# Kernel optimization log

Measured on AMD Instinct MI355X. Metric: run time of the kernel, lower is better.

Reference implementation:

```python
import jax, jax.numpy as jnp
import numpy as np

EPS = 1e-8


def setup_inputs() -> dict:
    key = jax.random.key(0)
    k1, k2, k3 = jax.random.split(key, 3)
    B, N_in, C = 4, 49152, 64   # 12*4^6 source cells
    N_out, K = 196608, 4        # 12*4^7 target cells, 4 IDW neighbors
    x = jax.random.normal(k1, (B, N_in, C), dtype=jnp.float32)
    nn_idx = jax.random.randint(k2, (N_out, K), 0, N_in, dtype=jnp.int64)
    nn_dist = jax.random.uniform(k3, (N_out, K), dtype=jnp.float32)
    return {"x": x, "nn_idx": nn_idx, "nn_dist": nn_dist}


def reference(x, nn_idx, nn_dist):
    # Inverse-distance weights over K nearest neighbors, normalized per target cell.
    inv = 1.0 / (nn_dist + EPS)                      # [N_out, K]
    w = inv / jnp.sum(inv, axis=-1, keepdims=True)   # [N_out, K]
    gathered = x[:, nn_idx, :]                       # [B, N_out, K, C] gather along source cells
    out = jnp.einsum("bnkc,nk->bnc", gathered, w)    # weighted reduce over neighbors
    return out
```

## Files before the change

kernel.cpp:

```cpp
#include <hip/hip_runtime.h>


#define IWD_EPS 1e-8f

typedef float f32x4 __attribute__((ext_vector_type(4)));
typedef int   i32x4 __attribute__((ext_vector_type(4)));
typedef unsigned int u32x4 __attribute__((ext_vector_type(4)));
typedef unsigned int u32x2 __attribute__((ext_vector_type(2)));

__device__ __forceinline__ float bf16lo_to_f32(unsigned int v) {
    unsigned int b = v << 16;
    return __builtin_bit_cast(float, b);
}
__device__ __forceinline__ float bf16hi_to_f32(unsigned int v) {
    unsigned int b = v & 0xFFFF0000u;
    return __builtin_bit_cast(float, b);
}
__device__ __forceinline__ unsigned int f32_to_bf16_rne(float f) {
    unsigned int u = __builtin_bit_cast(unsigned int, f);
    u += 0x7FFFu + ((u >> 16) & 1u);
    return u >> 16;
}

__global__ __launch_bounds__(256) void iwd_convert_bf16_kernel(
    const float* __restrict__ x, unsigned short* __restrict__ xb16, int nvec8)
{
    const int i = blockIdx.x * blockDim.x + threadIdx.x;
    if (i >= nvec8) return;
    const f32x4 a = *reinterpret_cast<const f32x4*>(x + (size_t)i * 8);
    const f32x4 b = *reinterpret_cast<const f32x4*>(x + (size_t)i * 8 + 4);
    u32x4 p;
    p.x = f32_to_bf16_rne(a.x) | (f32_to_bf16_rne(a.y) << 16);
    p.y = f32_to_bf16_rne(a.z) | (f32_to_bf16_rne(a.w) << 16);
    p.z = f32_to_bf16_rne(b.x) | (f32_to_bf16_rne(b.y) << 16);
    p.w = f32_to_bf16_rne(b.z) | (f32_to_bf16_rne(b.w) << 16);
    __builtin_nontemporal_store(p, reinterpret_cast<u32x4*>(xb16 + (size_t)i * 8));
}

__global__ __launch_bounds__(256) void IWD_ProjLayer_65876208386401_kernel(
    const unsigned short* __restrict__ xb16,
    const int*   __restrict__ nn_idx,
    const float* __restrict__ nn_dist,
    float* __restrict__ out)
{
    constexpr int N_in  = 49152;
    constexpr int C     = 64;
    constexpr int N_out = 196608;

    const int bid   = blockIdx.x;
    const int xcd   = bid & 7;
    const int b     = xcd >> 1;
    const int chunk = ((bid >> 3) << 1) | (xcd & 1);

    const int n  = chunk * 16 + (threadIdx.x >> 4);
    const int cq = (threadIdx.x & 15) * 4;

    const f32x4 d4 = *reinterpret_cast<const f32x4*>(nn_dist + (size_t)n * 4);
    const i32x4 id = *reinterpret_cast<const i32x4*>(nn_idx + (size_t)n * 4);

    const float i0 = 1.0f / (d4.x + IWD_EPS);
    const float i1 = 1.0f / (d4.y + IWD_EPS);
    const float i2 = 1.0f / (d4.z + IWD_EPS);
    const float i3 = 1.0f / (d4.w + IWD_EPS);
    const float r  = 1.0f / (i0 + i1 + i2 + i3);
    const float w0 = i0 * r, w1 = i1 * r, w2 = i2 * r, w3 = i3 * r;

    const unsigned short* xb = xb16 + (size_t)b * N_in * C;
    const u32x2 a0 = *reinterpret_cast<const u32x2*>(xb + (size_t)id.x * C + cq);
    const u32x2 a1 = *reinterpret_cast<const u32x2*>(xb + (size_t)id.y * C + cq);
    const u32x2 a2 = *reinterpret_cast<const u32x2*>(xb + (size_t)id.z * C + cq);
    const u32x2 a3 = *reinterpret_cast<const u32x2*>(xb + (size_t)id.w * C + cq);

    f32x4 o;
    o.x = bf16lo_to_f32(a0.x) * w0 + bf16lo_to_f32(a1.x) * w1
        + bf16lo_to_f32(a2.x) * w2 + bf16lo_to_f32(a3.x) * w3;
    o.y = bf16hi_to_f32(a0.x) * w0 + bf16hi_to_f32(a1.x) * w1
        + bf16hi_to_f32(a2.x) * w2 + bf16hi_to_f32(a3.x) * w3;
    o.z = bf16lo_to_f32(a0.y) * w0 + bf16lo_to_f32(a1.y) * w1
        + bf16lo_to_f32(a2.y) * w2 + bf16lo_to_f32(a3.y) * w3;
    o.w = bf16hi_to_f32(a0.y) * w0 + bf16hi_to_f32(a1.y) * w1
        + bf16hi_to_f32(a2.y) * w2 + bf16hi_to_f32(a3.y) * w3;

    __builtin_nontemporal_store(
        o, reinterpret_cast<f32x4*>(out + ((size_t)b * N_out + n) * C + cq));
}

__global__ __launch_bounds__(256) void iwd_f32_fallback_kernel(
    const float* __restrict__ x, const int* __restrict__ nn_idx,
    const float* __restrict__ nn_dist, float* __restrict__ out)
{
    constexpr int N_in = 49152, C = 64, N_out = 196608;
    const int bid = blockIdx.x, xcd = bid & 7, b = xcd >> 1;
    const int chunk = ((bid >> 3) << 1) | (xcd & 1);
    const int n  = chunk * 16 + (threadIdx.x >> 4);
    const int cq = (threadIdx.x & 15) * 4;

    const f32x4 d4 = *reinterpret_cast<const f32x4*>(nn_dist + (size_t)n * 4);
    const i32x4 id = *reinterpret_cast<const i32x4*>(nn_idx + (size_t)n * 4);
    const float i0 = 1.0f / (d4.x + IWD_EPS), i1 = 1.0f / (d4.y + IWD_EPS);
    const float i2 = 1.0f / (d4.z + IWD_EPS), i3 = 1.0f / (d4.w + IWD_EPS);
    const float r = 1.0f / (i0 + i1 + i2 + i3);
    const float w0 = i0 * r, w1 = i1 * r, w2 = i2 * r, w3 = i3 * r;

    const float* xb = x + (size_t)b * N_in * C;
    const f32x4 a0 = *reinterpret_cast<const f32x4*>(xb + (size_t)id.x * C + cq);
    const f32x4 a1 = *reinterpret_cast<const f32x4*>(xb + (size_t)id.y * C + cq);
    const f32x4 a2 = *reinterpret_cast<const f32x4*>(xb + (size_t)id.z * C + cq);
    const f32x4 a3 = *reinterpret_cast<const f32x4*>(xb + (size_t)id.w * C + cq);
    const f32x4 o = a0 * w0 + a1 * w1 + a2 * w2 + a3 * w3;
    __builtin_nontemporal_store(
        o, reinterpret_cast<f32x4*>(out + ((size_t)b * N_out + n) * C + cq));
}

extern "C" void kernel_launch(void* const* d_in, const int* in_sizes, int n_in,
                              void* d_out, int out_size, void* d_ws, size_t ws_size,
                              hipStream_t stream) {
    const float* x       = (const float*)d_in[0];
    const int*   nn_idx  = (const int*)d_in[1];
    const float* nn_dist = (const float*)d_in[2];
    float*       out     = (float*)d_out;

    constexpr int B = 4, N_in = 49152, C = 64, N_out = 196608;
    constexpr size_t XB16_BYTES = (size_t)B * N_in * C * 2;

    const int grid_main = (N_out / 16) * B;

    if (ws_size >= XB16_BYTES) {
        unsigned short* xb16 = (unsigned short*)d_ws;
        const int nvec8 = B * N_in * C / 8;
        iwd_convert_bf16_kernel<<<(nvec8 + 255) / 256, 256, 0, stream>>>(x, xb16, nvec8);
        IWD_ProjLayer_65876208386401_kernel<<<grid_main, 256, 0, stream>>>(xb16, nn_idx, nn_dist, out);
    } else {
        iwd_f32_fallback_kernel<<<grid_main, 256, 0, stream>>>(x, nn_idx, nn_dist, out);
    }
}
```

Measured before the change: 84.22 us.

## Split bf16 source into per-XCD channel-half planes to shrink gather working set

The conversion kernel now writes the bf16 copy of x as separate planes per (batch, channel-half), each row 32 channels (64 bytes). The gather kernel assigns each XCD one batch and one channel half, with 8 threads per target cell covering 32 channels and 32 cells per block. The aim is to halve the source working set each XCD touches so its L2 holds it better and the random gathers hit more often. In exchange each gathered row is only 64 bytes, and each cell's nn_idx/nn_dist are read by two XCDs instead of one.

```diff
diff --git a/kernel.cpp b/kernel.cpp
--- a/kernel.cpp
+++ b/kernel.cpp
@@ -9,12 +9,10 @@
 typedef unsigned int u32x2 __attribute__((ext_vector_type(2)));
 
 __device__ __forceinline__ float bf16lo_to_f32(unsigned int v) {
-    unsigned int b = v << 16;
-    return __builtin_bit_cast(float, b);
+    return __builtin_bit_cast(float, v << 16);
 }
 __device__ __forceinline__ float bf16hi_to_f32(unsigned int v) {
-    unsigned int b = v & 0xFFFF0000u;
-    return __builtin_bit_cast(float, b);
+    return __builtin_bit_cast(float, v & 0xFFFF0000u);
 }
 __device__ __forceinline__ unsigned int f32_to_bf16_rne(float f) {
     unsigned int u = __builtin_bit_cast(unsigned int, f);
@@ -22,38 +20,49 @@
     return u >> 16;
 }
 
-__global__ __launch_bounds__(256) void iwd_convert_bf16_kernel(
-    const float* __restrict__ x, unsigned short* __restrict__ xb16, int nvec8)
+__global__ __launch_bounds__(256) void iwd_convert_split_kernel(
+    const float* __restrict__ x, unsigned short* __restrict__ xs, int nvec8)
 {
+    constexpr int N_in = 49152;
     const int i = blockIdx.x * blockDim.x + threadIdx.x;
     if (i >= nvec8) return;
+
+    const int c    = (i * 8) & 63;
+    const int rowb = (i * 8) >> 6;
+    const int h    = c >> 5;
+    const int c32  = c & 31;
+    const int b    = rowb / N_in;
+    const int row  = rowb - b * N_in;
+
     const f32x4 a = *reinterpret_cast<const f32x4*>(x + (size_t)i * 8);
-    const f32x4 b = *reinterpret_cast<const f32x4*>(x + (size_t)i * 8 + 4);
+    const f32x4 d = *reinterpret_cast<const f32x4*>(x + (size_t)i * 8 + 4);
     u32x4 p;
     p.x = f32_to_bf16_rne(a.x) | (f32_to_bf16_rne(a.y) << 16);
     p.y = f32_to_bf16_rne(a.z) | (f32_to_bf16_rne(a.w) << 16);
-    p.z = f32_to_bf16_rne(b.x) | (f32_to_bf16_rne(b.y) << 16);
-    p.w = f32_to_bf16_rne(b.z) | (f32_to_bf16_rne(b.w) << 16);
-    __builtin_nontemporal_store(p, reinterpret_cast<u32x4*>(xb16 + (size_t)i * 8));
+    p.z = f32_to_bf16_rne(d.x) | (f32_to_bf16_rne(d.y) << 16);
+    p.w = f32_to_bf16_rne(d.z) | (f32_to_bf16_rne(d.w) << 16);
+
+    unsigned short* dst = xs + (((size_t)(b * 2 + h) * N_in + row) * 32 + c32);
+    __builtin_nontemporal_store(p, reinterpret_cast<u32x4*>(dst));
 }
 
 __global__ __launch_bounds__(256) void IWD_ProjLayer_65876208386401_kernel(
-    const unsigned short* __restrict__ xb16,
+    const unsigned short* __restrict__ xs,
     const int*   __restrict__ nn_idx,
     const float* __restrict__ nn_dist,
     float* __restrict__ out)
 {
     constexpr int N_in  = 49152;
-    constexpr int C     = 64;
     constexpr int N_out = 196608;
 
     const int bid   = blockIdx.x;
     const int xcd   = bid & 7;
     const int b     = xcd >> 1;
-    const int chunk = ((bid >> 3) << 1) | (xcd & 1);
+    const int h     = xcd & 1;
+    const int chunk = bid >> 3;
 
-    const int n  = chunk * 16 + (threadIdx.x >> 4);
-    const int cq = (threadIdx.x & 15) * 4;
+    const int n   = chunk * 32 + (threadIdx.x >> 3);
+    const int c32 = (threadIdx.x & 7) * 4;
 
     const f32x4 d4 = *reinterpret_cast<const f32x4*>(nn_dist + (size_t)n * 4);
     const i32x4 id = *reinterpret_cast<const i32x4*>(nn_idx + (size_t)n * 4);
@@ -65,11 +74,11 @@
     const float r  = 1.0f / (i0 + i1 + i2 + i3);
     const float w0 = i0 * r, w1 = i1 * r, w2 = i2 * r, w3 = i3 * r;
 
-    const unsigned short* xb = xb16 + (size_t)b * N_in * C;
-    const u32x2 a0 = *reinterpret_cast<const u32x2*>(xb + (size_t)id.x * C + cq);
-    const u32x2 a1 = *reinterpret_cast<const u32x2*>(xb + (size_t)id.y * C + cq);
-    const u32x2 a2 = *reinterpret_cast<const u32x2*>(xb + (size_t)id.z * C + cq);
-    const u32x2 a3 = *reinterpret_cast<const u32x2*>(xb + (size_t)id.w * C + cq);
+    const unsigned short* plane = xs + (size_t)(b * 2 + h) * N_in * 32;
+    const u32x2 a0 = *reinterpret_cast<const u32x2*>(plane + id.x * 32 + c32);
+    const u32x2 a1 = *reinterpret_cast<const u32x2*>(plane + id.y * 32 + c32);
+    const u32x2 a2 = *reinterpret_cast<const u32x2*>(plane + id.z * 32 + c32);
+    const u32x2 a3 = *reinterpret_cast<const u32x2*>(plane + id.w * 32 + c32);
 
     f32x4 o;
     o.x = bf16lo_to_f32(a0.x) * w0 + bf16lo_to_f32(a1.x) * w1
@@ -81,8 +90,8 @@
     o.w = bf16hi_to_f32(a0.y) * w0 + bf16hi_to_f32(a1.y) * w1
         + bf16hi_to_f32(a2.y) * w2 + bf16hi_to_f32(a3.y) * w3;
 
-    __builtin_nontemporal_store(
-        o, reinterpret_cast<f32x4*>(out + ((size_t)b * N_out + n) * C + cq));
+    float* op = out + ((size_t)b * N_out + n) * 64 + h * 32 + c32;
+    __builtin_nontemporal_store(o, reinterpret_cast<f32x4*>(op));
 }
 
 __global__ __launch_bounds__(256) void iwd_f32_fallback_kernel(
@@ -121,16 +130,16 @@
     float*       out     = (float*)d_out;
 
     constexpr int B = 4, N_in = 49152, C = 64, N_out = 196608;
-    constexpr size_t XB16_BYTES = (size_t)B * N_in * C * 2;
+    constexpr size_t XS_BYTES = (size_t)B * N_in * C * 2;
 
-    const int grid_main = (N_out / 16) * B;
-
-    if (ws_size >= XB16_BYTES) {
-        unsigned short* xb16 = (unsigned short*)d_ws;
+    if (ws_size >= XS_BYTES) {
+        unsigned short* xs = (unsigned short*)d_ws;
         const int nvec8 = B * N_in * C / 8;
-        iwd_convert_bf16_kernel<<<(nvec8 + 255) / 256, 256, 0, stream>>>(x, xb16, nvec8);
-        IWD_ProjLayer_65876208386401_kernel<<<grid_main, 256, 0, stream>>>(xb16, nn_idx, nn_dist, out);
+        iwd_convert_split_kernel<<<(nvec8 + 255) / 256, 256, 0, stream>>>(x, xs, nvec8);
+        const int grid = (N_out / 32) * B * 2;
+        IWD_ProjLayer_65876208386401_kernel<<<grid, 256, 0, stream>>>(xs, nn_idx, nn_dist, out);
     } else {
-        iwd_f32_fallback_kernel<<<grid_main, 256, 0, stream>>>(x, nn_idx, nn_dist, out);
+        const int grid = (N_out / 16) * B;
+        iwd_f32_fallback_kernel<<<grid, 256, 0, stream>>>(x, nn_idx, nn_dist, out);
     }
 }
```

Result: faster. 77.12 us (-8.4%).
